# Optimization experiments

Measured on AMD Instinct MI355X. Metric: run time of the kernel, lower is better.

The kernel has to match this reference:

```python
import jax, jax.numpy as jnp
import numpy as np

C, H, W, D, M = 64, 512, 512, 4, 16


def setup_inputs() -> dict:
    key = jax.random.key(0)
    ks = jax.random.split(key, 9)
    scale = (1.0 / (C * C)) ** 0.5
    return {
        "q": jax.random.normal(ks[0], (1, 1, H, W), jnp.float32),
        "proj_w": jax.random.normal(ks[1], (C, 1, 1, 1), jnp.float32),
        "proj_b": jax.random.normal(ks[2], (C, 1, 1), jnp.float32) * 0.01,
        "spec_wr": jax.random.normal(ks[3], (D, C, C, M, M), jnp.float32) * scale,
        "spec_wi": jax.random.normal(ks[4], (D, C, C, M, M), jnp.float32) * scale,
        "w_w": jax.random.normal(ks[5], (D, C, C, 1, 1), jnp.float32) * (1.0 / C ** 0.5),
        "w_b": jax.random.normal(ks[6], (D, C, 1, 1), jnp.float32) * 0.01,
        "final_w": jax.random.normal(ks[7], (1, C, 1, 1), jnp.float32) * (1.0 / C ** 0.5),
        "final_b": jax.random.normal(ks[8], (1, 1, 1), jnp.float32) * 0.01,
    }


def _spectral(x, wr, wi, m):
    # x: (C,H,W). FFT2 -> contract low modes -> zero-pad -> iFFT2, take real part.
    Cin, Hh, Ww = x.shape
    x_ft = jnp.fft.fft2(x, axes=(-2, -1))  # (C,H,W) complex
    w = (wr + 1j * wi).astype(x_ft.dtype)  # (Cin,Cout,m,m)
    out_sub = jnp.einsum('imn,iomn->omn', x_ft[:, :m, :m], w)
    out_ft = jnp.zeros((wr.shape[1], Hh, Ww), dtype=x_ft.dtype).at[:, :m, :m].set(out_sub)
    return jnp.fft.ifft2(out_ft, axes=(-2, -1)).real


def reference(q, proj_w, proj_b, spec_wr, spec_wi, w_w, w_b, final_w, final_b):
    m = spec_wr.shape[-1]
    depth = spec_wr.shape[0]
    x = q[0].astype(jnp.float32)  # (C_in,H,W) -- batch must be 1
    # 1x1 conv lift
    x = jnp.einsum('oi,ihw->ohw', proj_w[:, :, 0, 0], x) + proj_b
    for d in range(depth):
        x_spec = _spectral(x, spec_wr[d], spec_wi[d], m)
        x_local = jnp.einsum('oi,ihw->ohw', w_w[d, :, :, 0, 0], x) + w_b[d]
        x = jax.nn.gelu(x_spec + x_local)
    x = jnp.einsum('oi,ihw->ohw', final_w[:, :, 0, 0], x) + final_b
    return x[None]  # re-add batch dim
```

## Files before the change

kernel.cpp:

```cpp
#include <hip/hip_runtime.h>
#include <cmath>

#define CC 64
#define HH 512
#define WWID 512
#define HWSZ (HH*WWID)
#define DEPTH 4

typedef __attribute__((ext_vector_type(8))) short short8;
typedef __attribute__((ext_vector_type(4))) float floatx4;

__device__ inline unsigned short f2bf(float f){
  unsigned int u = __float_as_uint(f);
  u += 0x7FFF + ((u >> 16) & 1);
  return (unsigned short)(u >> 16);
}
__device__ inline float bf2f(unsigned short h){
  return __uint_as_float(((unsigned int)h) << 16);
}

__global__ void k_init(const float* __restrict__ ww,
                       float* __restrict__ ctab, float* __restrict__ stab,
                       unsigned short* __restrict__ trigBh, unsigned short* __restrict__ trigBl,
                       unsigned short* __restrict__ trigTh, unsigned short* __restrict__ trigTl,
                       unsigned short* __restrict__ Whi, unsigned short* __restrict__ Wlo){
  int idx = blockIdx.x*256 + threadIdx.x;
  if (idx < 8192){
    int pos = idx >> 4, k = idx & 15;
    int r = (pos * k) & 511;
    double ang = (2.0 * 3.14159265358979323846 / 512.0) * (double)r;
    float c = (float)cos(ang), s = (float)sin(ang);
    ctab[idx] = c;  stab[idx] = s;
    unsigned short ch = f2bf(c), sh = f2bf(s);
    unsigned short cl = f2bf(c - bf2f(ch)), sl = f2bf(s - bf2f(sh));
    trigBh[pos*32 + 2*k]     = ch;  trigBl[pos*32 + 2*k]     = cl;
    trigBh[pos*32 + 2*k + 1] = sh;  trigBl[pos*32 + 2*k + 1] = sl;
    trigTh[(2*k)*512 + pos]   = ch;  trigTl[(2*k)*512 + pos]   = cl;
    trigTh[(2*k+1)*512 + pos] = sh;  trigTl[(2*k+1)*512 + pos] = sl;
  } else {
    int t = idx - 8192;
    float v = ww[t];
    unsigned short h = f2bf(v);
    Whi[t] = h;  Wlo[t] = f2bf(v - bf2f(h));
  }
}

__global__ void k_lift(const float4* __restrict__ q, const float* __restrict__ pw,
                       const float* __restrict__ pb, float4* __restrict__ x,
                       float4* __restrict__ Xfz){
  if (blockIdx.x < 32) Xfz[blockIdx.x*256 + threadIdx.x] = make_float4(0.f,0.f,0.f,0.f);
  int idx = blockIdx.x*256 + threadIdx.x;
  int c = idx >> 16, p = idx & (HWSZ/4 - 1);
  float4 v = q[p];
  float a = pw[c], b = pb[c];
  v.x = fmaf(a, v.x, b); v.y = fmaf(a, v.y, b);
  v.z = fmaf(a, v.z, b); v.w = fmaf(a, v.w, b);
  x[idx] = v;
}

#define APITCH 136
#define XPITCH 33
__global__ __launch_bounds__(256) void k_dftw(const float* __restrict__ x,
    const unsigned short* __restrict__ trigTh, const unsigned short* __restrict__ trigTl,
    const float* __restrict__ ctab, const float* __restrict__ stab,
    float* __restrict__ Xfa, float4* __restrict__ Yz){
  if (blockIdx.x < 32) Yz[blockIdx.x*256 + threadIdx.x] = make_float4(0.f,0.f,0.f,0.f);

  __shared__ unsigned short Ahs[64*APITCH], Als[64*APITCH];
  __shared__ unsigned short Bhs[32*APITCH], Bls[32*APITCH];
  __shared__ float X1s[64*XPITCH];
  int row0 = blockIdx.x * 64;
  int i  = row0 >> 9;
  int h0 = row0 & 511;
  int t = threadIdx.x;
  int g = t >> 6, lm = t & 15, lq = (t >> 4) & 3;

  floatx4 acc[2] = {{0.f,0.f,0.f,0.f},{0.f,0.f,0.f,0.f}};

  for (int kc = 0; kc < 4; ++kc){
    {
      int r = t >> 2, q = t & 3;
      const float4* src4 = (const float4*)(x + (size_t)(row0 + r)*512 + kc*128 + q*32);
      unsigned int* dh = (unsigned int*)&Ahs[r*APITCH + q*32];
      unsigned int* dl = (unsigned int*)&Als[r*APITCH + q*32];
      #pragma unroll
      for (int u = 0; u < 8; ++u){
        float4 v = src4[u];
        unsigned short h0_ = f2bf(v.x), h1 = f2bf(v.y), h2 = f2bf(v.z), h3 = f2bf(v.w);
        dh[u*2]   = (unsigned)h0_ | ((unsigned)h1 << 16);
        dh[u*2+1] = (unsigned)h2 | ((unsigned)h3 << 16);
        unsigned short g0 = f2bf(v.x - bf2f(h0_)), g1 = f2bf(v.y - bf2f(h1));
        unsigned short g2 = f2bf(v.z - bf2f(h2)), g3 = f2bf(v.w - bf2f(h3));
        dl[u*2]   = (unsigned)g0 | ((unsigned)g1 << 16);
        dl[u*2+1] = (unsigned)g2 | ((unsigned)g3 << 16);
      }
    }
    {
      int j = t >> 3, q = t & 7;
      const unsigned int* sh = (const unsigned int*)trigTh + j*256 + kc*64 + q*8;
      const unsigned int* sl = (const unsigned int*)trigTl + j*256 + kc*64 + q*8;
      unsigned int* dh = (unsigned int*)&Bhs[j*APITCH + q*16];
      unsigned int* dl = (unsigned int*)&Bls[j*APITCH + q*16];
      #pragma unroll
      for (int u = 0; u < 8; ++u){ dh[u] = sh[u]; dl[u] = sl[u]; }
    }
    __syncthreads();
    #pragma unroll
    for (int ks = 0; ks < 4; ++ks){
      short8 ah = *(const short8*)&Ahs[(g*16 + lm)*APITCH + ks*32 + lq*8];
      short8 al = *(const short8*)&Als[(g*16 + lm)*APITCH + ks*32 + lq*8];
      #pragma unroll
      for (int nt = 0; nt < 2; ++nt){
        short8 bh = *(const short8*)&Bhs[(nt*16 + lm)*APITCH + ks*32 + lq*8];
        short8 bl = *(const short8*)&Bls[(nt*16 + lm)*APITCH + ks*32 + lq*8];
        acc[nt] = __builtin_amdgcn_mfma_f32_16x16x32_bf16(ah, bh, acc[nt], 0, 0, 0);
        acc[nt] = __builtin_amdgcn_mfma_f32_16x16x32_bf16(ah, bl, acc[nt], 0, 0, 0);
        acc[nt] = __builtin_amdgcn_mfma_f32_16x16x32_bf16(al, bh, acc[nt], 0, 0, 0);
      }
    }
    __syncthreads();
  }
  #pragma unroll
  for (int nt = 0; nt < 2; ++nt){
    int j = nt*16 + lm;
    float sgn = (j & 1) ? -1.f : 1.f;
    #pragma unroll
    for (int rg = 0; rg < 4; ++rg){
      int m = g*16 + lq*4 + rg;
      X1s[m*XPITCH + j] = sgn * acc[nt][rg];
    }
  }
  __syncthreads();

  int mo = t >> 4, n = t & 15;
  float ar = 0.f, ai = 0.f;
  #pragma unroll 8
  for (int hh = 0; hh < 64; ++hh){
    int h = h0 + hh;
    float Re = X1s[hh*XPITCH + 2*n];
    float Im = X1s[hh*XPITCH + 2*n + 1];
    float c = ctab[h*16 + mo], s = stab[h*16 + mo];
    ar += Re*c + Im*s;
    ai += Im*c - Re*s;
  }
  atomicAdd(&Xfa[(i*256 + t)*2],     ar);
  atomicAdd(&Xfa[(i*256 + t)*2 + 1], ai);
}

__global__ void k_contract(const float2* __restrict__ Xf,
                           const float* __restrict__ wr, const float* __restrict__ wi,
                           float* __restrict__ Ya){
  int o = blockIdx.x, ic = blockIdx.y;
  int mn = blockIdx.z*64 + threadIdx.x;
  float ar = 0.f, ai = 0.f;
  int i0 = ic * 16;
  #pragma unroll
  for (int ii = 0; ii < 16; ++ii){
    int i = i0 + ii;
    float2 xf = Xf[i*256 + mn];
    float wrv = wr[(i*64 + o)*256 + mn];
    float wiv = wi[(i*64 + o)*256 + mn];
    ar += xf.x*wrv - xf.y*wiv;
    ai += xf.x*wiv + xf.y*wrv;
  }
  const float sc = 1.f/262144.f;
  atomicAdd(&Ya[(o*256 + mn)*2],     ar*sc);
  atomicAdd(&Ya[(o*256 + mn)*2 + 1], ai*sc);
}

__global__ void k_idfth(const float2* __restrict__ Y, const float* __restrict__ ct,
                        const float* __restrict__ st,
                        unsigned int* __restrict__ Thi, unsigned int* __restrict__ Tlo,
                        float4* __restrict__ Xfz){
  if (blockIdx.x < 32) Xfz[blockIdx.x*256 + threadIdx.x] = make_float4(0.f,0.f,0.f,0.f);
  int idx = blockIdx.x*256 + threadIdx.x;
  int n = idx & 15, o = (idx >> 4) & 63, h = idx >> 10;
  float ar = 0.f, ai = 0.f;
  #pragma unroll
  for (int m = 0; m < 16; ++m){
    float2 y = Y[(o<<8) + (m<<4) + n];
    float c = ct[h*16 + m], s = st[h*16 + m];
    ar += y.x*c - y.y*s;
    ai += y.x*s + y.y*c;
  }
  float tr = ar, ts = -ai;
  unsigned short rh = f2bf(tr), sh = f2bf(ts);
  Thi[idx] = (unsigned int)rh | ((unsigned int)sh << 16);
  unsigned short rl = f2bf(tr - bf2f(rh)), slr = f2bf(ts - bf2f(sh));
  Tlo[idx] = (unsigned int)rl | ((unsigned int)slr << 16);
}

#define PITCH 104
__global__ __launch_bounds__(256) void k_combine(
    const float* __restrict__ x,
    const unsigned short* __restrict__ Whid, const unsigned short* __restrict__ Wlod,
    const unsigned int* __restrict__ Thi,  const unsigned int* __restrict__ Tlo,
    const unsigned short* __restrict__ trigBh, const unsigned short* __restrict__ trigBl,
    const float* __restrict__ wb, float* __restrict__ xo)
{
  __shared__ unsigned short Ah[64*PITCH], Al[64*PITCH];
  __shared__ unsigned short Bh[64*PITCH], Bl[64*PITCH];
  int h  = blockIdx.y;
  int w0 = blockIdx.x * 64;
  int t  = threadIdx.x;

  {
    int wl = t & 63, ig = t >> 6;
    const float* xb = x + (size_t)h*512 + w0 + wl;
    #pragma unroll
    for (int ii = 0; ii < 16; ii += 2){
      int i0 = ig*16 + ii;
      float v0 = xb[(size_t)i0*HWSZ];
      float v1 = xb[(size_t)(i0+1)*HWSZ];
      unsigned short h0 = f2bf(v0), h1 = f2bf(v1);
      unsigned short g0 = f2bf(v0 - bf2f(h0)), g1 = f2bf(v1 - bf2f(h1));
      *(unsigned int*)&Bh[wl*PITCH + i0] = (unsigned int)h0 | ((unsigned int)h1 << 16);
      *(unsigned int*)&Bl[wl*PITCH + i0] = (unsigned int)g0 | ((unsigned int)g1 << 16);
    }
  }
  {
    int row = t >> 2, qq = t & 3;
    const unsigned int* sh = (const unsigned int*)trigBh + (size_t)(w0+row)*16 + qq*4;
    const unsigned int* sl = (const unsigned int*)trigBl + (size_t)(w0+row)*16 + qq*4;
    unsigned int* dh = (unsigned int*)&Bh[row*PITCH + 64] + qq*4;
    unsigned int* dl = (unsigned int*)&Bl[row*PITCH + 64] + qq*4;
    #pragma unroll
    for (int u = 0; u < 4; ++u){ dh[u] = sh[u]; dl[u] = sl[u]; }
  }
  {
    int o = t >> 2, q8 = t & 3;
    const unsigned int* sh = (const unsigned int*)Whid + o*32 + q8*8;
    const unsigned int* sl = (const unsigned int*)Wlod + o*32 + q8*8;
    unsigned int* dh = (unsigned int*)&Ah[o*PITCH] + q8*8;
    unsigned int* dl = (unsigned int*)&Al[o*PITCH] + q8*8;
    #pragma unroll
    for (int u = 0; u < 8; ++u){ dh[u] = sh[u]; dl[u] = sl[u]; }
  }
  {
    int o = t >> 2, q4 = t & 3;
    const unsigned int* sh = Thi + (size_t)h*1024 + o*16 + q4*4;
    const unsigned int* sl = Tlo + (size_t)h*1024 + o*16 + q4*4;
    unsigned int* dh = (unsigned int*)&Ah[o*PITCH + 64] + q4*4;
    unsigned int* dl = (unsigned int*)&Al[o*PITCH + 64] + q4*4;
    #pragma unroll
    for (int u = 0; u < 4; ++u){ dh[u] = sh[u]; dl[u] = sl[u]; }
  }
  __syncthreads();

  int g  = t >> 6;
  int lm = t & 15;
  int lq = (t >> 4) & 3;

  floatx4 acc[4] = {{0.f,0.f,0.f,0.f},{0.f,0.f,0.f,0.f},{0.f,0.f,0.f,0.f},{0.f,0.f,0.f,0.f}};

  #pragma unroll
  for (int ks = 0; ks < 3; ++ks){
    short8 af = *(const short8*)&Ah[(g*16 + lm)*PITCH + ks*32 + lq*8];
    short8 al = *(const short8*)&Al[(g*16 + lm)*PITCH + ks*32 + lq*8];
    #pragma unroll
    for (int nt = 0; nt < 4; ++nt){
      short8 bf = *(const short8*)&Bh[(nt*16 + lm)*PITCH + ks*32 + lq*8];
      short8 bl = *(const short8*)&Bl[(nt*16 + lm)*PITCH + ks*32 + lq*8];
      acc[nt] = __builtin_amdgcn_mfma_f32_16x16x32_bf16(af, bf, acc[nt], 0, 0, 0);
      acc[nt] = __builtin_amdgcn_mfma_f32_16x16x32_bf16(af, bl, acc[nt], 0, 0, 0);
      acc[nt] = __builtin_amdgcn_mfma_f32_16x16x32_bf16(al, bf, acc[nt], 0, 0, 0);
    }
  }

  #pragma unroll
  for (int nt = 0; nt < 4; ++nt){
    int w = w0 + nt*16 + lm;
    #pragma unroll
    for (int rg = 0; rg < 4; ++rg){
      int o = g*16 + lq*4 + rg;
      float u = acc[nt][rg] + wb[o];
      float z = 0.7978845608028654f * fmaf(0.044715f, u*u*u, u);
      float e = __expf(2.f*z);
      float gl = u - __fdividef(u, e + 1.f);
      xo[(size_t)o*HWSZ + (size_t)h*512 + w] = gl;
    }
  }
}

__global__ void k_final(const float* __restrict__ x, const float* __restrict__ fw,
                        const float* __restrict__ fb, float4* __restrict__ out){
  int p4 = blockIdx.x*256 + threadIdx.x;
  float b = fb[0];
  float4 acc = make_float4(b, b, b, b);
  #pragma unroll
  for (int i = 0; i < CC; ++i){
    float4 v = *(const float4*)(x + (size_t)i*HWSZ + (size_t)p4*4);
    float wv = fw[i];
    acc.x = fmaf(wv, v.x, acc.x); acc.y = fmaf(wv, v.y, acc.y);
    acc.z = fmaf(wv, v.z, acc.z); acc.w = fmaf(wv, v.w, acc.w);
  }
  out[p4] = acc;
}

extern "C" void kernel_launch(void* const* d_in, const int* in_sizes, int n_in,
                              void* d_out, int out_size, void* d_ws, size_t ws_size,
                              hipStream_t stream) {
  const float* q       = (const float*)d_in[0];
  const float* proj_w  = (const float*)d_in[1];
  const float* proj_b  = (const float*)d_in[2];
  const float* spec_wr = (const float*)d_in[3];
  const float* spec_wi = (const float*)d_in[4];
  const float* w_w     = (const float*)d_in[5];
  const float* w_b     = (const float*)d_in[6];
  const float* final_w = (const float*)d_in[7];
  const float* final_b = (const float*)d_in[8];
  float* out = (float*)d_out;

  char* ws = (char*)d_ws;
  float*  ctab = (float*) (ws + 0);
  float*  stab = (float*) (ws + 32768);
  unsigned short* trigBh = (unsigned short*)(ws + 65536);
  unsigned short* trigBl = (unsigned short*)(ws + 98304);
  unsigned int* Thi = (unsigned int*)(ws + 131072);
  unsigned int* Tlo = (unsigned int*)(ws + 2228224);
  float*  Xf   = (float*) (ws + 4325376);
  float*  Y    = (float*) (ws + 4456448);
  float*  x    = (float*) (ws + 4587520);
  unsigned short* Whi = (unsigned short*)(ws + 71696384);
  unsigned short* Wlo = (unsigned short*)(ws + 71729152);
  unsigned short* trigTh = (unsigned short*)(ws + 71761920);
  unsigned short* trigTl = (unsigned short*)(ws + 71794688);

  k_init<<<96, 256, 0, stream>>>(w_w, ctab, stab, trigBh, trigBl, trigTh, trigTl, Whi, Wlo);
  k_lift<<<16384, 256, 0, stream>>>((const float4*)q, proj_w, proj_b, (float4*)x,
                                    (float4*)Xf);

  for (int d = 0; d < DEPTH; ++d){
    k_dftw<<<512, 256, 0, stream>>>(x, trigTh, trigTl, ctab, stab, Xf, (float4*)Y);
    k_contract<<<dim3(64,4,4), 64, 0, stream>>>((const float2*)Xf,
                                                spec_wr + (size_t)d*1048576,
                                                spec_wi + (size_t)d*1048576, Y);
    k_idfth<<<2048, 256, 0, stream>>>((const float2*)Y, ctab, stab, Thi, Tlo,
                                      (float4*)Xf);
    k_combine<<<dim3(8,512), 256, 0, stream>>>(x, Whi + d*4096, Wlo + d*4096,
                                               Thi, Tlo, trigBh, trigBl,
                                               w_b + d*64, x);
  }
  k_final<<<256, 256, 0, stream>>>(x, final_w, final_b, (float4*)out);
}
```

Baseline: 348.0 us.

## Fuse lift into first DFT/combine and final projection into last combine

Removes the separate lift kernel by recomputing the 1x1 lift from q inside the first-layer DFT and combine kernels. It also folds the final channel reduction into the last combine kernel through a shared-memory reduction, so the last layer's 64-channel activation is never written and the final kernel is gone. This avoids writing and reading several full 64x512x512 fp32 tensors. The cost is two extra template variants and a small block-level reduction in the final combine.

After: 317.5 us. -8.8%, faster.

```diff
diff --git a/kernel.cpp b/kernel.cpp
--- a/kernel.cpp
+++ b/kernel.cpp
@@ -23,7 +23,9 @@
                        float* __restrict__ ctab, float* __restrict__ stab,
                        unsigned short* __restrict__ trigBh, unsigned short* __restrict__ trigBl,
                        unsigned short* __restrict__ trigTh, unsigned short* __restrict__ trigTl,
-                       unsigned short* __restrict__ Whi, unsigned short* __restrict__ Wlo){
+                       unsigned short* __restrict__ Whi, unsigned short* __restrict__ Wlo,
+                       float4* __restrict__ Xfz){
+  if (blockIdx.x < 32) Xfz[blockIdx.x*256 + threadIdx.x] = make_float4(0.f,0.f,0.f,0.f);
   int idx = blockIdx.x*256 + threadIdx.x;
   if (idx < 8192){
     int pos = idx >> 4, k = idx & 15;
@@ -45,22 +47,11 @@
   }
 }
 
-__global__ void k_lift(const float4* __restrict__ q, const float* __restrict__ pw,
-                       const float* __restrict__ pb, float4* __restrict__ x,
-                       float4* __restrict__ Xfz){
-  if (blockIdx.x < 32) Xfz[blockIdx.x*256 + threadIdx.x] = make_float4(0.f,0.f,0.f,0.f);
-  int idx = blockIdx.x*256 + threadIdx.x;
-  int c = idx >> 16, p = idx & (HWSZ/4 - 1);
-  float4 v = q[p];
-  float a = pw[c], b = pb[c];
-  v.x = fmaf(a, v.x, b); v.y = fmaf(a, v.y, b);
-  v.z = fmaf(a, v.z, b); v.w = fmaf(a, v.w, b);
-  x[idx] = v;
-}
-
 #define APITCH 136
 #define XPITCH 33
+template<int LIFT>
 __global__ __launch_bounds__(256) void k_dftw(const float* __restrict__ x,
+    const float* __restrict__ qsrc, const float* __restrict__ pw, const float* __restrict__ pb,
     const unsigned short* __restrict__ trigTh, const unsigned short* __restrict__ trigTl,
     const float* __restrict__ ctab, const float* __restrict__ stab,
     float* __restrict__ Xfa, float4* __restrict__ Yz){
@@ -74,18 +65,26 @@
   int h0 = row0 & 511;
   int t = threadIdx.x;
   int g = t >> 6, lm = t & 15, lq = (t >> 4) & 3;
+  float pa = 0.f, pbv = 0.f;
+  if (LIFT){ pa = pw[i]; pbv = pb[i]; }
 
   floatx4 acc[2] = {{0.f,0.f,0.f,0.f},{0.f,0.f,0.f,0.f}};
 
   for (int kc = 0; kc < 4; ++kc){
     {
-      int r = t >> 2, q = t & 3;
-      const float4* src4 = (const float4*)(x + (size_t)(row0 + r)*512 + kc*128 + q*32);
-      unsigned int* dh = (unsigned int*)&Ahs[r*APITCH + q*32];
-      unsigned int* dl = (unsigned int*)&Als[r*APITCH + q*32];
+      int r = t >> 2, qq = t & 3;
+      const float4* src4 = LIFT
+        ? (const float4*)(qsrc + (size_t)(h0 + r)*512 + kc*128 + qq*32)
+        : (const float4*)(x    + (size_t)(row0 + r)*512 + kc*128 + qq*32);
+      unsigned int* dh = (unsigned int*)&Ahs[r*APITCH + qq*32];
+      unsigned int* dl = (unsigned int*)&Als[r*APITCH + qq*32];
       #pragma unroll
       for (int u = 0; u < 8; ++u){
         float4 v = src4[u];
+        if (LIFT){
+          v.x = fmaf(pa, v.x, pbv); v.y = fmaf(pa, v.y, pbv);
+          v.z = fmaf(pa, v.z, pbv); v.w = fmaf(pa, v.w, pbv);
+        }
         unsigned short h0_ = f2bf(v.x), h1 = f2bf(v.y), h2 = f2bf(v.z), h3 = f2bf(v.w);
         dh[u*2]   = (unsigned)h0_ | ((unsigned)h1 << 16);
         dh[u*2+1] = (unsigned)h2 | ((unsigned)h3 << 16);
@@ -96,11 +95,11 @@
       }
     }
     {
-      int j = t >> 3, q = t & 7;
-      const unsigned int* sh = (const unsigned int*)trigTh + j*256 + kc*64 + q*8;
-      const unsigned int* sl = (const unsigned int*)trigTl + j*256 + kc*64 + q*8;
-      unsigned int* dh = (unsigned int*)&Bhs[j*APITCH + q*16];
-      unsigned int* dl = (unsigned int*)&Bls[j*APITCH + q*16];
+      int j = t >> 3, qq = t & 7;
+      const unsigned int* sh = (const unsigned int*)trigTh + j*256 + kc*64 + qq*8;
+      const unsigned int* sl = (const unsigned int*)trigTl + j*256 + kc*64 + qq*8;
+      unsigned int* dh = (unsigned int*)&Bhs[j*APITCH + qq*16];
+      unsigned int* dl = (unsigned int*)&Bls[j*APITCH + qq*16];
       #pragma unroll
       for (int u = 0; u < 8; ++u){ dh[u] = sh[u]; dl[u] = sl[u]; }
     }
@@ -191,12 +190,16 @@
 }
 
 #define PITCH 104
+template<int LIFT, int FINAL>
 __global__ __launch_bounds__(256) void k_combine(
-    const float* __restrict__ x,
+    const float* __restrict__ x, const float* __restrict__ qsrc,
+    const float* __restrict__ pw, const float* __restrict__ pb,
     const unsigned short* __restrict__ Whid, const unsigned short* __restrict__ Wlod,
     const unsigned int* __restrict__ Thi,  const unsigned int* __restrict__ Tlo,
     const unsigned short* __restrict__ trigBh, const unsigned short* __restrict__ trigBl,
-    const float* __restrict__ wb, float* __restrict__ xo)
+    const float* __restrict__ wb, float* __restrict__ xo,
+    const float* __restrict__ fw, const float* __restrict__ fb,
+    float* __restrict__ outp)
 {
   __shared__ unsigned short Ah[64*PITCH], Al[64*PITCH];
   __shared__ unsigned short Bh[64*PITCH], Bl[64*PITCH];
@@ -206,16 +209,30 @@
 
   {
     int wl = t & 63, ig = t >> 6;
-    const float* xb = x + (size_t)h*512 + w0 + wl;
-    #pragma unroll
-    for (int ii = 0; ii < 16; ii += 2){
-      int i0 = ig*16 + ii;
-      float v0 = xb[(size_t)i0*HWSZ];
-      float v1 = xb[(size_t)(i0+1)*HWSZ];
-      unsigned short h0 = f2bf(v0), h1 = f2bf(v1);
-      unsigned short g0 = f2bf(v0 - bf2f(h0)), g1 = f2bf(v1 - bf2f(h1));
-      *(unsigned int*)&Bh[wl*PITCH + i0] = (unsigned int)h0 | ((unsigned int)h1 << 16);
-      *(unsigned int*)&Bl[wl*PITCH + i0] = (unsigned int)g0 | ((unsigned int)g1 << 16);
+    if (LIFT){
+      float qv = qsrc[(size_t)h*512 + w0 + wl];
+      #pragma unroll
+      for (int ii = 0; ii < 16; ii += 2){
+        int i0 = ig*16 + ii;
+        float v0 = fmaf(pw[i0],   qv, pb[i0]);
+        float v1 = fmaf(pw[i0+1], qv, pb[i0+1]);
+        unsigned short h0 = f2bf(v0), h1 = f2bf(v1);
+        unsigned short g0 = f2bf(v0 - bf2f(h0)), g1 = f2bf(v1 - bf2f(h1));
+        *(unsigned int*)&Bh[wl*PITCH + i0] = (unsigned int)h0 | ((unsigned int)h1 << 16);
+        *(unsigned int*)&Bl[wl*PITCH + i0] = (unsigned int)g0 | ((unsigned int)g1 << 16);
+      }
+    } else {
+      const float* xb = x + (size_t)h*512 + w0 + wl;
+      #pragma unroll
+      for (int ii = 0; ii < 16; ii += 2){
+        int i0 = ig*16 + ii;
+        float v0 = xb[(size_t)i0*HWSZ];
+        float v1 = xb[(size_t)(i0+1)*HWSZ];
+        unsigned short h0 = f2bf(v0), h1 = f2bf(v1);
+        unsigned short g0 = f2bf(v0 - bf2f(h0)), g1 = f2bf(v1 - bf2f(h1));
+        *(unsigned int*)&Bh[wl*PITCH + i0] = (unsigned int)h0 | ((unsigned int)h1 << 16);
+        *(unsigned int*)&Bl[wl*PITCH + i0] = (unsigned int)g0 | ((unsigned int)g1 << 16);
+      }
     }
   }
   {
@@ -267,34 +284,44 @@
     }
   }
 
-  #pragma unroll
-  for (int nt = 0; nt < 4; ++nt){
-    int w = w0 + nt*16 + lm;
-    #pragma unroll
-    for (int rg = 0; rg < 4; ++rg){
-      int o = g*16 + lq*4 + rg;
-      float u = acc[nt][rg] + wb[o];
-      float z = 0.7978845608028654f * fmaf(0.044715f, u*u*u, u);
-      float e = __expf(2.f*z);
-      float gl = u - __fdividef(u, e + 1.f);
-      xo[(size_t)o*HWSZ + (size_t)h*512 + w] = gl;
-    }
-  }
-}
-
-__global__ void k_final(const float* __restrict__ x, const float* __restrict__ fw,
-                        const float* __restrict__ fb, float4* __restrict__ out){
-  int p4 = blockIdx.x*256 + threadIdx.x;
-  float b = fb[0];
-  float4 acc = make_float4(b, b, b, b);
-  #pragma unroll
-  for (int i = 0; i < CC; ++i){
-    float4 v = *(const float4*)(x + (size_t)i*HWSZ + (size_t)p4*4);
-    float wv = fw[i];
-    acc.x = fmaf(wv, v.x, acc.x); acc.y = fmaf(wv, v.y, acc.y);
-    acc.z = fmaf(wv, v.z, acc.z); acc.w = fmaf(wv, v.w, acc.w);
-  }
-  out[p4] = acc;
+  if (!FINAL){
+    #pragma unroll
+    for (int nt = 0; nt < 4; ++nt){
+      int w = w0 + nt*16 + lm;
+      #pragma unroll
+      for (int rg = 0; rg < 4; ++rg){
+        int o = g*16 + lq*4 + rg;
+        float u = acc[nt][rg] + wb[o];
+        float z = 0.7978845608028654f * fmaf(0.044715f, u*u*u, u);
+        float e = __expf(2.f*z);
+        float gl = u - __fdividef(u, e + 1.f);
+        xo[(size_t)o*HWSZ + (size_t)h*512 + w] = gl;
+      }
+    }
+  } else {
+    __shared__ float fred[64*17];
+    #pragma unroll
+    for (int nt = 0; nt < 4; ++nt){
+      float partial = 0.f;
+      #pragma unroll
+      for (int rg = 0; rg < 4; ++rg){
+        int o = g*16 + lq*4 + rg;
+        float u = acc[nt][rg] + wb[o];
+        float z = 0.7978845608028654f * fmaf(0.044715f, u*u*u, u);
+        float e = __expf(2.f*z);
+        float gl = u - __fdividef(u, e + 1.f);
+        partial = fmaf(fw[o], gl, partial);
+      }
+      fred[(nt*16 + lm)*17 + (t >> 4)] = partial;
+    }
+    __syncthreads();
+    if (t < 64){
+      float s = fb[0];
+      #pragma unroll
+      for (int k2 = 0; k2 < 16; ++k2) s += fred[t*17 + k2];
+      outp[(size_t)h*512 + w0 + t] = s;
+    }
+  }
 }
 
 extern "C" void kernel_launch(void* const* d_in, const int* in_sizes, int n_in,
@@ -326,20 +353,32 @@
   unsigned short* trigTh = (unsigned short*)(ws + 71761920);
   unsigned short* trigTl = (unsigned short*)(ws + 71794688);
 
-  k_init<<<96, 256, 0, stream>>>(w_w, ctab, stab, trigBh, trigBl, trigTh, trigTl, Whi, Wlo);
-  k_lift<<<16384, 256, 0, stream>>>((const float4*)q, proj_w, proj_b, (float4*)x,
-                                    (float4*)Xf);
+  k_init<<<96, 256, 0, stream>>>(w_w, ctab, stab, trigBh, trigBl, trigTh, trigTl,
+                                 Whi, Wlo, (float4*)Xf);
 
   for (int d = 0; d < DEPTH; ++d){
-    k_dftw<<<512, 256, 0, stream>>>(x, trigTh, trigTl, ctab, stab, Xf, (float4*)Y);
+    if (d == 0)
+      k_dftw<1><<<512, 256, 0, stream>>>(x, q, proj_w, proj_b, trigTh, trigTl,
+                                         ctab, stab, Xf, (float4*)Y);
+    else
+      k_dftw<0><<<512, 256, 0, stream>>>(x, q, proj_w, proj_b, trigTh, trigTl,
+                                         ctab, stab, Xf, (float4*)Y);
     k_contract<<<dim3(64,4,4), 64, 0, stream>>>((const float2*)Xf,
                                                 spec_wr + (size_t)d*1048576,
                                                 spec_wi + (size_t)d*1048576, Y);
     k_idfth<<<2048, 256, 0, stream>>>((const float2*)Y, ctab, stab, Thi, Tlo,
                                       (float4*)Xf);
-    k_combine<<<dim3(8,512), 256, 0, stream>>>(x, Whi + d*4096, Wlo + d*4096,
-                                               Thi, Tlo, trigBh, trigBl,
-                                               w_b + d*64, x);
-  }
-  k_final<<<256, 256, 0, stream>>>(x, final_w, final_b, (float4*)out);
-}
+    if (d == 0)
+      k_combine<1,0><<<dim3(8,512), 256, 0, stream>>>(x, q, proj_w, proj_b,
+          Whi + d*4096, Wlo + d*4096, Thi, Tlo, trigBh, trigBl,
+          w_b + d*64, x, final_w, final_b, out);
+    else if (d < DEPTH-1)
+      k_combine<0,0><<<dim3(8,512), 256, 0, stream>>>(x, q, proj_w, proj_b,
+          Whi + d*4096, Wlo + d*4096, Thi, Tlo, trigBh, trigBl,
+          w_b + d*64, x, final_w, final_b, out);
+    else
+      k_combine<0,1><<<dim3(8,512), 256, 0, stream>>>(x, q, proj_w, proj_b,
+          Whi + d*4096, Wlo + d*4096, Thi, Tlo, trigBh, trigBl,
+          w_b + d*64, x, final_w, final_b, out);
+  }
+}
```
